# Optimization experiments

Hardware: AMD Instinct MI355X
Metric: run time of the kernel (lower is better)

The kernel has to match this reference:

```python
import jax, jax.numpy as jnp
import numpy as np

EPS = 1e-5  # nn.LayerNorm default

def _ln(x, g, b):
    m = x.mean(-1, keepdims=True)
    v = ((x - m) ** 2).mean(-1, keepdims=True)
    return (x - m) / jnp.sqrt(v + EPS) * g + b


def setup_inputs() -> dict:
    key = jax.random.key(0)
    ks = jax.random.split(key, 16)
    B, T, H, W = 8, 20, 224, 224
    D, NC = 1536, 7
    s = 0.02
    f32 = jnp.float32
    return {
        'x': jax.random.normal(ks[0], (B, 3, T, H, W), f32),
        'timestamp': jax.random.uniform(ks[1], (B,), f32),
        # surrogate backbone: patchify conv (stride 16) + global avg pool -> 1536 feats
        'conv_w': jax.random.normal(ks[2], (D, 3, 16, 16), f32) * s,
        'conv_b': jnp.zeros((D,), f32),
        'w_red': jax.random.normal(ks[3], (D, D), f32) * s,
        'b_red': jnp.zeros((D,), f32),
        'w_num': jax.random.normal(ks[4], (D, 1), f32) * s,
        'b_num': jnp.zeros((D,), f32),
        'time_embed': jax.random.normal(ks[5], (1, T, D), f32) * s,
        'cls_swap': jax.random.normal(ks[6], (1, 5, 1, D), f32) * s,
        'ln_g': jnp.ones((D,), f32),
        'ln_b': jnp.zeros((D,), f32),
        'w_qkv': jax.random.normal(ks[7], (3 * D, D), f32) * s,
        'w_tproj': jax.random.normal(ks[8], (D, D), f32) * s,
        'b_tproj': jnp.zeros((D,), f32),
        'w_tfc': jax.random.normal(ks[9], (D, D), f32) * s,
        'b_tfc': jnp.zeros((D,), f32),
        'w_head': jax.random.normal(ks[10], (NC, D), f32) * s,
        'b_head': jnp.zeros((NC,), f32),
    }


def reference(x, timestamp, conv_w, conv_b, w_red, b_red, w_num, b_num,
              time_embed, cls_swap, ln_g, ln_b, w_qkv, w_tproj, b_tproj,
              w_tfc, b_tfc, w_head, b_head):
    B, C, T, H, W = x.shape
    D = w_red.shape[0]
    NH = 12
    HD = D // NH
    scale = HD ** -0.5

    # (b t) c h w  -> backbone surrogate -> (B*T, D)
    xf = jnp.transpose(x, (0, 2, 1, 3, 4)).reshape(B * T, C, H, W)
    f = jax.lax.conv_general_dilated(
        xf, conv_w, window_strides=(16, 16), padding='VALID',
        dimension_numbers=('NCHW', 'OIHW', 'NCHW'))
    f = (f + conv_b[None, :, None, None]).mean((2, 3))  # global avg pool -> (BT, D)

    xr = (f @ w_red.T + b_red).reshape(B, T, D)           # reduce_dim
    xt = xr + time_embed
    te = timestamp[:, None] @ w_num.T + b_num             # NumberToVector (B, D)
    xt = xt + te[:, None, :]

    # groups: b (n k) c -> b n k c, k=4, n=5; prepend 1 cls token per group
    g = jnp.concatenate(
        [jnp.broadcast_to(cls_swap, (B, 5, 1, D)), xt.reshape(B, 5, 4, D)], axis=2)

    for _ in range(4):  # num_interactions
        gr = g.reshape(B * 5, 5, D)
        hn = _ln(gr, ln_g, ln_b)
        qkv = (hn @ w_qkv.T).reshape(B * 5, 5, 3, NH, HD).transpose(2, 0, 3, 1, 4)
        q, k, v = qkv[0], qkv[1], qkv[2]                  # (b*n, h, t, hd)
        a = jax.nn.softmax(jnp.einsum('bhqd,bhkd->bhqk', q, k) * scale, axis=-1)
        o = jnp.einsum('bhqk,bhkd->bhqd', a, v).transpose(0, 2, 1, 3).reshape(B * 5, 5, D)
        o = o @ w_tproj.T + b_tproj                       # attn proj
        upd = (o @ w_tfc.T + b_tfc) + gr                  # temporal_fc + residual
        g = upd.reshape(B, 5, 5, D)
        # swap cls tokens between groups via roll
        g = g.at[:, :, 0, :].set(jnp.roll(g[:, :, 0, :], 1, axis=1))

    xt = g[:, :, 1:, :].reshape(B, T, D)
    out = xt[:, -1, :] + xr[:, -1, :]
    return out @ w_head.T + b_head  # (B, num_classes)
```

## Files before the change

### kernel.cpp

```cpp
#include <hip/hip_runtime.h>

typedef __attribute__((ext_vector_type(8))) short short8;
typedef __attribute__((ext_vector_type(8))) unsigned short ushort8;
typedef __attribute__((ext_vector_type(4))) float f32x4;
typedef unsigned short ushort_t;

__device__ __forceinline__ ushort_t f2bf(float f) {
    unsigned u = __builtin_bit_cast(unsigned, f);
    u += 0x7fffu + ((u >> 16) & 1u);
    return (ushort_t)(u >> 16);
}
__device__ __forceinline__ float bf2f(ushort_t u) {
    unsigned v = ((unsigned)u) << 16;
    return __builtin_bit_cast(float, v);
}

__device__ __forceinline__ void load_lds16(const void* gp, void* lp) {
    __builtin_amdgcn_global_load_lds(
        (const __attribute__((address_space(1))) void*)gp,
        (__attribute__((address_space(3))) void*)lp, 16, 0, 0);
}

__global__ __launch_bounds__(256, 4) void pool_kernel(
    const float* __restrict__ x, ushort_t* __restrict__ AP) {
    int blk = blockIdx.x, tid = threadIdx.x;
    int bt = blk / 12, rc = blk % 12;
    int c = rc >> 2, igrp = rc & 3;
    int w = tid >> 6, lane = tid & 63;
    int i = igrp * 4 + w;
    int b = bt / 20, t = bt % 20;
    const float* base = x + (size_t)((b * 3 + c) * 20 + t) * 50176;

    f32x4 v[13];
    int ri = (lane >= 56) ? 1 : 0;
    int c4 = lane - 56 * ri;
    #pragma unroll
    for (int it = 0; it < 13; ++it) {
        if (it < 12 || lane < 16)
            v[it] = *(const f32x4*)(base + (16 * ri + i) * 224 + 4 * c4);
        else
            v[it] = (f32x4){0.f, 0.f, 0.f, 0.f};
        ri += 1; c4 += 8;
        if (c4 >= 56) { c4 -= 56; ri += 1; }
    }
    #pragma unroll
    for (int s = 1; s < 13; s <<= 1)
        #pragma unroll
        for (int j = 0; j + s < 13; j += 2 * s)
            v[j] += v[j + s];
    f32x4 acc = v[0];
    #pragma unroll
    for (int m = 4; m <= 32; m <<= 1) {
        acc[0] += __shfl_xor(acc[0], m);
        acc[1] += __shfl_xor(acc[1], m);
        acc[2] += __shfl_xor(acc[2], m);
        acc[3] += __shfl_xor(acc[3], m);
    }
    if (lane < 4) {
        ushort4 o;
        o.x = f2bf(acc[0] * (1.f / 196.f));
        o.y = f2bf(acc[1] * (1.f / 196.f));
        o.z = f2bf(acc[2] * (1.f / 196.f));
        o.w = f2bf(acc[3] * (1.f / 196.f));
        *(ushort4*)(AP + (size_t)bt * 768 + c * 256 + i * 16 + 4 * lane) = o;
    }
}

__global__ __launch_bounds__(256) void wprep_kernel(
    const float* __restrict__ w_qkv, const float* __restrict__ w_tf,
    const float* __restrict__ w_red, const float* __restrict__ conv_w,
    const float* __restrict__ w_tp, const float* __restrict__ b_tp,
    const float* __restrict__ b_tf, const float* __restrict__ cls,
    ushort_t* __restrict__ WQ, ushort_t* __restrict__ WF,
    ushort_t* __restrict__ WR, ushort_t* __restrict__ WCV,
    ushort_t* __restrict__ WTT, float* __restrict__ BC,
    float* __restrict__ GA) {
    __shared__ __align__(16) float smem[64 * 68];
    int blk = blockIdx.x, tid = threadIdx.x;
    if (blk < 6336) {
        long c = (long)blk * 256 + tid;
        const float* s; ushort_t* d; long i;
        if (c < 884736)       { s = w_qkv;  d = WQ;  i = c; }
        else if (c < 1179648) { s = w_tf;   d = WF;  i = c - 884736; }
        else if (c < 1474560) { s = w_red;  d = WR;  i = c - 1179648; }
        else                  { s = conv_w; d = WCV; i = c - 1474560; }
        i <<= 3;
        f32x4 a = *(const f32x4*)(s + i);
        f32x4 b = *(const f32x4*)(s + i + 4);
        ushort8 o;
        o[0] = f2bf(a[0]); o[1] = f2bf(a[1]); o[2] = f2bf(a[2]); o[3] = f2bf(a[3]);
        o[4] = f2bf(b[0]); o[5] = f2bf(b[1]); o[6] = f2bf(b[2]); o[7] = f2bf(b[3]);
        *(ushort8*)(d + i) = o;
    } else if (blk < 6912) {
        int tb = blk - 6336;
        int bi = tb / 24, bj = tb % 24;
        int r0 = (tid >> 4) << 2;
        int c0 = (tid & 15) << 2;
        #pragma unroll
        for (int rr = 0; rr < 4; ++rr) {
            f32x4 v = *(const f32x4*)(w_tp + (size_t)(bi * 64 + r0 + rr) * 1536 + bj * 64 + c0);
            smem[(r0 + rr) * 68 + c0 + 0] = v[0];
            smem[(r0 + rr) * 68 + c0 + 1] = v[1];
            smem[(r0 + rr) * 68 + c0 + 2] = v[2];
            smem[(r0 + rr) * 68 + c0 + 3] = v[3];
        }
        __syncthreads();
        #pragma unroll
        for (int rr = 0; rr < 4; ++rr) {
            int jj = r0 + rr;
            ushort4 o;
            o.x = f2bf(smem[(c0 + 0) * 68 + jj]);
            o.y = f2bf(smem[(c0 + 1) * 68 + jj]);
            o.z = f2bf(smem[(c0 + 2) * 68 + jj]);
            o.w = f2bf(smem[(c0 + 3) * 68 + jj]);
            *(ushort4*)(WTT + (size_t)(bj * 64 + jj) * 1536 + bi * 64 + c0) = o;
        }
    } else if (blk < 6952) {
        int cblk = blk - 6912;
        int b = cblk / 5, n = cblk % 5;
        size_t row = (size_t)(b * 25 + n * 5) * 1536;
        #pragma unroll
        for (int j = 0; j < 6; ++j) {
            int d = tid + j * 256;
            GA[row + d] = cls[n * 1536 + d];
        }
    } else {
        int bb = blk - 6952;
        int row = bb * 16 + (tid >> 4);
        int sub = tid & 15;
        float acc = 0.f;
        for (int j = 0; j < 96; ++j) {
            int k = sub + j * 16;
            acc += w_tf[(size_t)row * 1536 + k] * b_tp[k];
        }
        acc += __shfl_xor(acc, 1); acc += __shfl_xor(acc, 2);
        acc += __shfl_xor(acc, 4); acc += __shfl_xor(acc, 8);
        if (sub == 0) BC[row] = acc + b_tf[row];
    }
}

template <int MT, bool OUT_BF16, bool HAS_BIAS, bool HAS_RES, bool CLS_SWAP, bool BUILD_G>
__global__ __launch_bounds__(64) void gemm_kernel(
    const ushort_t* __restrict__ A, const ushort_t* __restrict__ B,
    void* __restrict__ Cv, const float* __restrict__ bias,
    const float* __restrict__ res, int M, int N, int K,
    float* __restrict__ g_out, const float* __restrict__ temb,
    const float* __restrict__ ts, const float* __restrict__ w_num,
    const float* __restrict__ b_num) {
    constexpr int BUFB = MT * 2048 + 8192;
    __shared__ __align__(16) char lds[2 * BUFB];
    const int lane = threadIdx.x;
    const int tn = blockIdx.x, tm = blockIdx.y;

    f32x4 acc[MT][4];
    #pragma unroll
    for (int m = 0; m < MT; ++m)
        #pragma unroll
        for (int n = 0; n < 4; ++n)
            acc[m][n] = (f32x4){0.f, 0.f, 0.f, 0.f};

    const int nK = K >> 6;
    const int rbase = lane >> 3, cc = lane & 7;

    auto stage = [&](int k0, int buf) {
        char* lA = lds + buf * BUFB;
        char* lB = lA + MT * 2048;
        #pragma unroll
        for (int j = 0; j < MT * 2; ++j) {
            int row = j * 8 + rbase;
            int cf = cc ^ (row & 7);
            int ga = tm * (MT * 16) + row; if (ga > M - 1) ga = M - 1;
            load_lds16(A + (size_t)ga * K + (k0 + cf * 8), lA + j * 1024);
        }
        #pragma unroll
        for (int j = 0; j < 8; ++j) {
            int row = j * 8 + rbase;
            int cf = cc ^ (row & 7);
            load_lds16(B + (size_t)(tn * 64 + row) * K + (k0 + cf * 8), lB + j * 1024);
        }
    };

    stage(0, 0);
    for (int t = 0; t < nK; ++t) {
        int cur = t & 1;
        if (t + 1 < nK) {
            stage((t + 1) << 6, cur ^ 1);
            if constexpr (MT == 2) asm volatile("s_waitcnt vmcnt(12)" ::: "memory");
            else                   asm volatile("s_waitcnt vmcnt(16)" ::: "memory");
        } else {
            asm volatile("s_waitcnt vmcnt(0)" ::: "memory");
        }
        __builtin_amdgcn_sched_barrier(0);
        const char* lA = lds + cur * BUFB;
        const char* lB = lA + MT * 2048;
        #pragma unroll
        for (int ks = 0; ks < 2; ++ks) {
            short8 av[MT], bv[4];
            const int rlo = lane & 15;
            const int chi = ks * 4 + (lane >> 4);
            #pragma unroll
            for (int m = 0; m < MT; ++m) {
                int r = m * 16 + rlo;
                av[m] = *(const short8*)(lA + r * 128 + ((chi ^ (r & 7)) << 4));
            }
            #pragma unroll
            for (int n = 0; n < 4; ++n) {
                int r = n * 16 + rlo;
                bv[n] = *(const short8*)(lB + r * 128 + ((chi ^ (r & 7)) << 4));
            }
            #pragma unroll
            for (int m = 0; m < MT; ++m)
                #pragma unroll
                for (int n = 0; n < 4; ++n)
                    acc[m][n] = __builtin_amdgcn_mfma_f32_16x16x32_bf16(
                        av[m], bv[n], acc[m][n], 0, 0, 0);
        }
    }

    const int c_l = lane & 15, r_q = (lane >> 4) * 4;
    #pragma unroll
    for (int m = 0; m < MT; ++m) {
        #pragma unroll
        for (int reg = 0; reg < 4; ++reg) {
            int r_ = tm * (MT * 16) + m * 16 + r_q + reg;
            if (r_ < M) {
                int r2 = r_;
                if (CLS_SWAP) {
                    int bb = r_ / 25, rem = r_ % 25;
                    if (rem % 5 == 0) r2 = bb * 25 + ((rem / 5 + 1) % 5) * 5;
                }
                #pragma unroll
                for (int n = 0; n < 4; ++n) {
                    int cc_ = tn * 64 + n * 16 + c_l;
                    float v = acc[m][n][reg];
                    if (HAS_BIAS) v += bias[cc_];
                    if (HAS_RES) v += res[(size_t)r_ * N + cc_];
                    if (OUT_BF16) ((ushort_t*)Cv)[(size_t)r2 * N + cc_] = f2bf(v);
                    else          ((float*)Cv)[(size_t)r2 * N + cc_] = v;
                    if (BUILD_G) {
                        int b = r_ / 20, t = r_ % 20;
                        float gval = v + temb[t * 1536 + cc_] +
                                     ts[b] * w_num[cc_] + b_num[cc_];
                        g_out[(size_t)(b * 25 + (t / 4) * 5 + (t % 4) + 1) * 1536 + cc_] = gval;
                    }
                }
            }
        }
    }
}

__global__ __launch_bounds__(256) void ln_kernel(
    const float* __restrict__ g, const float* __restrict__ gamma,
    const float* __restrict__ beta, ushort_t* __restrict__ hn) {
    int r = blockIdx.x, tid = threadIdx.x;
    const float* x = g + (size_t)r * 1536;
    float v[6], s = 0.f, s2 = 0.f;
    #pragma unroll
    for (int j = 0; j < 6; ++j) {
        v[j] = x[tid + j * 256];
        s += v[j]; s2 += v[j] * v[j];
    }
    #pragma unroll
    for (int m = 1; m < 64; m <<= 1) { s += __shfl_xor(s, m); s2 += __shfl_xor(s2, m); }
    __shared__ float red[8];
    int wid = tid >> 6;
    if ((tid & 63) == 0) { red[wid] = s; red[4 + wid] = s2; }
    __syncthreads();
    s  = red[0] + red[1] + red[2] + red[3];
    s2 = red[4] + red[5] + red[6] + red[7];
    float mean = s * (1.0f / 1536.0f);
    float var  = s2 * (1.0f / 1536.0f) - mean * mean;
    float rstd = rsqrtf(var + 1e-5f);
    #pragma unroll
    for (int j = 0; j < 6; ++j) {
        int d = tid + j * 256;
        float y = (v[j] - mean) * rstd * gamma[d] + beta[d];
        hn[(size_t)r * 1536 + d] = f2bf(y);
    }
}

__global__ __launch_bounds__(64) void attn_kernel(const ushort_t* __restrict__ qkv,
                                                  ushort_t* __restrict__ o) {
    int gid = blockIdx.x;
    int h = gid % 12, gg = gid / 12;
    int l = threadIdx.x;
    const ushort_t* basep = qkv + (size_t)gg * 5 * 4608 + h * 128 + 2 * l;
    float q[5][2], k[5][2], v[5][2];
    #pragma unroll
    for (int tt = 0; tt < 5; ++tt) {
        ushort2 qv = *(const ushort2*)(basep + tt * 4608);
        ushort2 kv = *(const ushort2*)(basep + tt * 4608 + 1536);
        ushort2 vv = *(const ushort2*)(basep + tt * 4608 + 3072);
        q[tt][0] = bf2f(qv.x); q[tt][1] = bf2f(qv.y);
        k[tt][0] = bf2f(kv.x); k[tt][1] = bf2f(kv.y);
        v[tt][0] = bf2f(vv.x); v[tt][1] = bf2f(vv.y);
    }
    float sc[5][5];
    #pragma unroll
    for (int i = 0; i < 5; ++i)
        #pragma unroll
        for (int j = 0; j < 5; ++j)
            sc[i][j] = q[i][0] * k[j][0] + q[i][1] * k[j][1];
    #pragma unroll
    for (int m = 1; m < 64; m <<= 1)
        #pragma unroll
        for (int i = 0; i < 5; ++i)
            #pragma unroll
            for (int j = 0; j < 5; ++j)
                sc[i][j] += __shfl_xor(sc[i][j], m);
    const float scale = 0.08838834764831845f;
    float a_[5][5];
    #pragma unroll
    for (int i = 0; i < 5; ++i) {
        float mx = -1e30f;
        #pragma unroll
        for (int j = 0; j < 5; ++j) mx = fmaxf(mx, sc[i][j]);
        float sum = 0.f;
        #pragma unroll
        for (int j = 0; j < 5; ++j) { a_[i][j] = __expf((sc[i][j] - mx) * scale); sum += a_[i][j]; }
        float inv = 1.0f / sum;
        #pragma unroll
        for (int j = 0; j < 5; ++j) a_[i][j] *= inv;
    }
    #pragma unroll
    for (int i = 0; i < 5; ++i) {
        float o0 = 0.f, o1 = 0.f;
        #pragma unroll
        for (int j = 0; j < 5; ++j) { o0 += a_[i][j] * v[j][0]; o1 += a_[i][j] * v[j][1]; }
        ushort2 w; w.x = f2bf(o0); w.y = f2bf(o1);
        *(ushort2*)(o + (size_t)(gg * 5 + i) * 1536 + h * 128 + 2 * l) = w;
    }
}

__global__ __launch_bounds__(64) void head_kernel(
    const float* __restrict__ gfin, const float* __restrict__ xr,
    const float* __restrict__ w_head, const float* __restrict__ b_head,
    float* __restrict__ out) {
    int b = blockIdx.x, l = threadIdx.x;
    const float* gv = gfin + (size_t)(b * 25 + 24) * 1536;
    const float* xv = xr + (size_t)(b * 20 + 19) * 1536;
    float acc[7] = {0, 0, 0, 0, 0, 0, 0};
    for (int d = l; d < 1536; d += 64) {
        float xval = gv[d] + xv[d];
        #pragma unroll
        for (int c = 0; c < 7; ++c) acc[c] += xval * w_head[c * 1536 + d];
    }
    #pragma unroll
    for (int c = 0; c < 7; ++c)
        #pragma unroll
        for (int m = 1; m < 64; m <<= 1) acc[c] += __shfl_xor(acc[c], m);
    if (l == 0) {
        #pragma unroll
        for (int c = 0; c < 7; ++c) out[b * 7 + c] = acc[c] + b_head[c];
    }
}

#define OFF_WQ   0u
#define OFF_WF   14155776u
#define OFF_WR   18874368u
#define OFF_WCV  23592960u
#define OFF_WTT  25952256u
#define OFF_WC   30670848u
#define OFF_BC   35389440u
#define OFF_AP   35395584u
#define OFF_FBF  35641344u
#define OFF_XR   36132864u
#define OFF_GA   37115904u
#define OFF_GB   38344704u
#define OFF_HN   39573504u
#define OFF_QKV  40187904u
#define OFF_OBF  42031104u

extern "C" void kernel_launch(void* const* d_in, const int* in_sizes, int n_in,
                              void* d_out, int out_size, void* d_ws, size_t ws_size,
                              hipStream_t stream) {
    const float* x      = (const float*)d_in[0];
    const float* ts     = (const float*)d_in[1];
    const float* conv_w = (const float*)d_in[2];
    const float* conv_b = (const float*)d_in[3];
    const float* w_red  = (const float*)d_in[4];
    const float* b_red  = (const float*)d_in[5];
    const float* w_num  = (const float*)d_in[6];
    const float* b_num  = (const float*)d_in[7];
    const float* temb   = (const float*)d_in[8];
    const float* cls    = (const float*)d_in[9];
    const float* ln_g   = (const float*)d_in[10];
    const float* ln_b   = (const float*)d_in[11];
    const float* w_qkv  = (const float*)d_in[12];
    const float* w_tp   = (const float*)d_in[13];
    const float* b_tp   = (const float*)d_in[14];
    const float* w_tf   = (const float*)d_in[15];
    const float* b_tf   = (const float*)d_in[16];
    const float* w_head = (const float*)d_in[17];
    const float* b_head = (const float*)d_in[18];

    char* ws = (char*)d_ws;
    ushort_t* WQ  = (ushort_t*)(ws + OFF_WQ);
    ushort_t* WF  = (ushort_t*)(ws + OFF_WF);
    ushort_t* WR  = (ushort_t*)(ws + OFF_WR);
    ushort_t* WCV = (ushort_t*)(ws + OFF_WCV);
    ushort_t* WTT = (ushort_t*)(ws + OFF_WTT);
    ushort_t* WC  = (ushort_t*)(ws + OFF_WC);
    float*    BC  = (float*)(ws + OFF_BC);
    ushort_t* AP  = (ushort_t*)(ws + OFF_AP);
    ushort_t* FBF = (ushort_t*)(ws + OFF_FBF);
    float*    XR  = (float*)(ws + OFF_XR);
    float*    GA  = (float*)(ws + OFF_GA);
    float*    GB  = (float*)(ws + OFF_GB);
    ushort_t* HN  = (ushort_t*)(ws + OFF_HN);
    ushort_t* QKV = (ushort_t*)(ws + OFF_QKV);
    ushort_t* OBF = (ushort_t*)(ws + OFF_OBF);

    pool_kernel<<<1920, 256, 0, stream>>>(x, AP);
    wprep_kernel<<<7048, 256, 0, stream>>>(w_qkv, w_tf, w_red, conv_w, w_tp,
                                           b_tp, b_tf, cls,
                                           WQ, WF, WR, WCV, WTT, BC, GA);
    gemm_kernel<4, true, false, false, false, false><<<dim3(24, 24), 64, 0, stream>>>(
        WF, WTT, WC, nullptr, nullptr, 1536, 1536, 1536,
        nullptr, nullptr, nullptr, nullptr, nullptr);
    gemm_kernel<2, true, true, false, false, false><<<dim3(24, 5), 64, 0, stream>>>(
        AP, WCV, FBF, conv_b, nullptr, 160, 1536, 768,
        nullptr, nullptr, nullptr, nullptr, nullptr);
    gemm_kernel<2, false, true, false, false, true><<<dim3(24, 5), 64, 0, stream>>>(
        FBF, WR, XR, b_red, nullptr, 160, 1536, 1536,
        GA, temb, ts, w_num, b_num);

    float* gsrc = GA;
    float* gdst = GB;
    for (int it = 0; it < 4; ++it) {
        ln_kernel<<<200, 256, 0, stream>>>(gsrc, ln_g, ln_b, HN);
        gemm_kernel<4, true, false, false, false, false><<<dim3(72, 4), 64, 0, stream>>>(
            HN, WQ, QKV, nullptr, nullptr, 200, 4608, 1536,
            nullptr, nullptr, nullptr, nullptr, nullptr);
        attn_kernel<<<480, 64, 0, stream>>>(QKV, OBF);
        gemm_kernel<2, false, true, true, true, false><<<dim3(24, 7), 64, 0, stream>>>(
            OBF, WC, gdst, BC, gsrc, 200, 1536, 1536,
            nullptr, nullptr, nullptr, nullptr, nullptr);
        float* tmp = gsrc; gsrc = gdst; gdst = tmp;
    }
    head_kernel<<<8, 64, 0, stream>>>(gsrc, XR, w_head, b_head, (float*)d_out);
}
```

Before: 231.6 us.

## Split-K the QKV GEMM into two fp32 halves summed in attention

The QKV projection GEMM now splits K=1536 into two halves across twice as many blocks. Each half writes fp32 partial outputs to separate buffers, and the attention kernel loads both and adds them. This doubles the grid of the small-M GEMM to fill more CUs, at the cost of extra fp32 traffic into attention. The pool kernel's load indexing is also rewritten to compute row and column per iteration with a multiply-shift divide.

```diff
diff --git a/kernel.cpp b/kernel.cpp
--- a/kernel.cpp
+++ b/kernel.cpp
@@ -32,16 +32,14 @@
     const float* base = x + (size_t)((b * 3 + c) * 20 + t) * 50176;
 
     f32x4 v[13];
-    int ri = (lane >= 56) ? 1 : 0;
-    int c4 = lane - 56 * ri;
     #pragma unroll
     for (int it = 0; it < 13; ++it) {
-        if (it < 12 || lane < 16)
-            v[it] = *(const f32x4*)(base + (16 * ri + i) * 224 + 4 * c4);
-        else
-            v[it] = (f32x4){0.f, 0.f, 0.f, 0.f};
-        ri += 1; c4 += 8;
-        if (c4 >= 56) { c4 -= 56; ri += 1; }
+        int k = lane + it * 64;
+        int kk = k < 784 ? k : 0;
+        int ri = (kk * 9363) >> 19;
+        int c4 = kk - ri * 56;
+        v[it] = *(const f32x4*)(base + (16 * ri + i) * 224 + 4 * c4);
+        if (k >= 784) v[it] = (f32x4){0.f, 0.f, 0.f, 0.f};
     }
     #pragma unroll
     for (int s = 1; s < 13; s <<= 1)
@@ -139,18 +137,26 @@
     }
 }
 
-template <int MT, bool OUT_BF16, bool HAS_BIAS, bool HAS_RES, bool CLS_SWAP, bool BUILD_G>
+template <int MT, bool OUT_BF16, bool HAS_BIAS, bool HAS_RES, bool CLS_SWAP,
+          bool BUILD_G, bool SPLITK>
 __global__ __launch_bounds__(64) void gemm_kernel(
     const ushort_t* __restrict__ A, const ushort_t* __restrict__ B,
-    void* __restrict__ Cv, const float* __restrict__ bias,
-    const float* __restrict__ res, int M, int N, int K,
+    void* __restrict__ Cv, void* __restrict__ Cv2,
+    const float* __restrict__ bias, const float* __restrict__ res,
+    int M, int N, int K, int KS,
     float* __restrict__ g_out, const float* __restrict__ temb,
     const float* __restrict__ ts, const float* __restrict__ w_num,
     const float* __restrict__ b_num) {
     constexpr int BUFB = MT * 2048 + 8192;
     __shared__ __align__(16) char lds[2 * BUFB];
     const int lane = threadIdx.x;
-    const int tn = blockIdx.x, tm = blockIdx.y;
+    const int tn = blockIdx.x;
+    int tm = blockIdx.y;
+    if (SPLITK) {
+        int half = tm >> 2;
+        tm &= 3;
+        if (half) { A += K; B += K; Cv = Cv2; }
+    }
 
     f32x4 acc[MT][4];
     #pragma unroll
@@ -170,13 +176,13 @@
             int row = j * 8 + rbase;
             int cf = cc ^ (row & 7);
             int ga = tm * (MT * 16) + row; if (ga > M - 1) ga = M - 1;
-            load_lds16(A + (size_t)ga * K + (k0 + cf * 8), lA + j * 1024);
+            load_lds16(A + (size_t)ga * KS + (k0 + cf * 8), lA + j * 1024);
         }
         #pragma unroll
         for (int j = 0; j < 8; ++j) {
             int row = j * 8 + rbase;
             int cf = cc ^ (row & 7);
-            load_lds16(B + (size_t)(tn * 64 + row) * K + (k0 + cf * 8), lB + j * 1024);
+            load_lds16(B + (size_t)(tn * 64 + row) * KS + (k0 + cf * 8), lB + j * 1024);
         }
     };
 
@@ -279,21 +285,27 @@
     }
 }
 
-__global__ __launch_bounds__(64) void attn_kernel(const ushort_t* __restrict__ qkv,
-                                                  ushort_t* __restrict__ o) {
+__global__ __launch_bounds__(64) void attn_kernel(
+    const float* __restrict__ qA, const float* __restrict__ qB,
+    ushort_t* __restrict__ o) {
     int gid = blockIdx.x;
     int h = gid % 12, gg = gid / 12;
     int l = threadIdx.x;
-    const ushort_t* basep = qkv + (size_t)gg * 5 * 4608 + h * 128 + 2 * l;
+    size_t off = (size_t)gg * 5 * 4608 + h * 128 + 2 * l;
+    const float* b0 = qA + off;
+    const float* b1 = qB + off;
     float q[5][2], k[5][2], v[5][2];
     #pragma unroll
     for (int tt = 0; tt < 5; ++tt) {
-        ushort2 qv = *(const ushort2*)(basep + tt * 4608);
-        ushort2 kv = *(const ushort2*)(basep + tt * 4608 + 1536);
-        ushort2 vv = *(const ushort2*)(basep + tt * 4608 + 3072);
-        q[tt][0] = bf2f(qv.x); q[tt][1] = bf2f(qv.y);
-        k[tt][0] = bf2f(kv.x); k[tt][1] = bf2f(kv.y);
-        v[tt][0] = bf2f(vv.x); v[tt][1] = bf2f(vv.y);
+        float2 q0 = *(const float2*)(b0 + tt * 4608);
+        float2 q1 = *(const float2*)(b1 + tt * 4608);
+        float2 k0 = *(const float2*)(b0 + tt * 4608 + 1536);
+        float2 k1 = *(const float2*)(b1 + tt * 4608 + 1536);
+        float2 v0 = *(const float2*)(b0 + tt * 4608 + 3072);
+        float2 v1 = *(const float2*)(b1 + tt * 4608 + 3072);
+        q[tt][0] = q0.x + q1.x; q[tt][1] = q0.y + q1.y;
+        k[tt][0] = k0.x + k1.x; k[tt][1] = k0.y + k1.y;
+        v[tt][0] = v0.x + v1.x; v[tt][1] = v0.y + v1.y;
     }
     float sc[5][5];
     #pragma unroll
@@ -355,21 +367,22 @@
     }
 }
 
-#define OFF_WQ   0u
-#define OFF_WF   14155776u
-#define OFF_WR   18874368u
-#define OFF_WCV  23592960u
-#define OFF_WTT  25952256u
-#define OFF_WC   30670848u
-#define OFF_BC   35389440u
-#define OFF_AP   35395584u
-#define OFF_FBF  35641344u
-#define OFF_XR   36132864u
-#define OFF_GA   37115904u
-#define OFF_GB   38344704u
-#define OFF_HN   39573504u
-#define OFF_QKV  40187904u
-#define OFF_OBF  42031104u
+#define OFF_WQ    0u
+#define OFF_WF    14155776u
+#define OFF_WR    18874368u
+#define OFF_WCV   23592960u
+#define OFF_WTT   25952256u
+#define OFF_WC    30670848u
+#define OFF_BC    35389440u
+#define OFF_AP    35395584u
+#define OFF_FBF   35641344u
+#define OFF_XR    36132864u
+#define OFF_GA    37115904u
+#define OFF_GB    38344704u
+#define OFF_HN    39573504u
+#define OFF_QKV0  40187904u
+#define OFF_QKV1  43874304u
+#define OFF_OBF   47560704u
 
 extern "C" void kernel_launch(void* const* d_in, const int* in_sizes, int n_in,
                               void* d_out, int out_size, void* d_ws, size_t ws_size,
@@ -395,46 +408,47 @@
     const float* b_head = (const float*)d_in[18];
 
     char* ws = (char*)d_ws;
-    ushort_t* WQ  = (ushort_t*)(ws + OFF_WQ);
-    ushort_t* WF  = (ushort_t*)(ws + OFF_WF);
-    ushort_t* WR  = (ushort_t*)(ws + OFF_WR);
-    ushort_t* WCV = (ushort_t*)(ws + OFF_WCV);
-    ushort_t* WTT = (ushort_t*)(ws + OFF_WTT);
-    ushort_t* WC  = (ushort_t*)(ws + OFF_WC);
-    float*    BC  = (float*)(ws + OFF_BC);
-    ushort_t* AP  = (ushort_t*)(ws + OFF_AP);
-    ushort_t* FBF = (ushort_t*)(ws + OFF_FBF);
-    float*    XR  = (float*)(ws + OFF_XR);
-    float*    GA  = (float*)(ws + OFF_GA);
-    float*    GB  = (float*)(ws + OFF_GB);
-    ushort_t* HN  = (ushort_t*)(ws + OFF_HN);
-    ushort_t* QKV = (ushort_t*)(ws + OFF_QKV);
-    ushort_t* OBF = (ushort_t*)(ws + OFF_OBF);
+    ushort_t* WQ   = (ushort_t*)(ws + OFF_WQ);
+    ushort_t* WF   = (ushort_t*)(ws + OFF_WF);
+    ushort_t* WR   = (ushort_t*)(ws + OFF_WR);
+    ushort_t* WCV  = (ushort_t*)(ws + OFF_WCV);
+    ushort_t* WTT  = (ushort_t*)(ws + OFF_WTT);
+    ushort_t* WC   = (ushort_t*)(ws + OFF_WC);
+    float*    BC   = (float*)(ws + OFF_BC);
+    ushort_t* AP   = (ushort_t*)(ws + OFF_AP);
+    ushort_t* FBF  = (ushort_t*)(ws + OFF_FBF);
+    float*    XR   = (float*)(ws + OFF_XR);
+    float*    GA   = (float*)(ws + OFF_GA);
+    float*    GB   = (float*)(ws + OFF_GB);
+    ushort_t* HN   = (ushort_t*)(ws + OFF_HN);
+    float*    QKV0 = (float*)(ws + OFF_QKV0);
+    float*    QKV1 = (float*)(ws + OFF_QKV1);
+    ushort_t* OBF  = (ushort_t*)(ws + OFF_OBF);
 
     pool_kernel<<<1920, 256, 0, stream>>>(x, AP);
     wprep_kernel<<<7048, 256, 0, stream>>>(w_qkv, w_tf, w_red, conv_w, w_tp,
                                            b_tp, b_tf, cls,
                                            WQ, WF, WR, WCV, WTT, BC, GA);
-    gemm_kernel<4, true, false, false, false, false><<<dim3(24, 24), 64, 0, stream>>>(
-        WF, WTT, WC, nullptr, nullptr, 1536, 1536, 1536,
+    gemm_kernel<4, true, false, false, false, false, false><<<dim3(24, 24), 64, 0, stream>>>(
+        WF, WTT, WC, nullptr, nullptr, nullptr, 1536, 1536, 1536, 1536,
         nullptr, nullptr, nullptr, nullptr, nullptr);
-    gemm_kernel<2, true, true, false, false, false><<<dim3(24, 5), 64, 0, stream>>>(
-        AP, WCV, FBF, conv_b, nullptr, 160, 1536, 768,
+    gemm_kernel<2, true, true, false, false, false, false><<<dim3(24, 5), 64, 0, stream>>>(
+        AP, WCV, FBF, nullptr, conv_b, nullptr, 160, 1536, 768, 768,
         nullptr, nullptr, nullptr, nullptr, nullptr);
-    gemm_kernel<2, false, true, false, false, true><<<dim3(24, 5), 64, 0, stream>>>(
-        FBF, WR, XR, b_red, nullptr, 160, 1536, 1536,
+    gemm_kernel<2, false, true, false, false, true, false><<<dim3(24, 5), 64, 0, stream>>>(
+        FBF, WR, XR, nullptr, b_red, nullptr, 160, 1536, 1536, 1536,
         GA, temb, ts, w_num, b_num);
 
     float* gsrc = GA;
     float* gdst = GB;
     for (int it = 0; it < 4; ++it) {
         ln_kernel<<<200, 256, 0, stream>>>(gsrc, ln_g, ln_b, HN);
-        gemm_kernel<4, true, false, false, false, false><<<dim3(72, 4), 64, 0, stream>>>(
-            HN, WQ, QKV, nullptr, nullptr, 200, 4608, 1536,
+        gemm_kernel<4, false, false, false, false, false, true><<<dim3(72, 8), 64, 0, stream>>>(
+            HN, WQ, QKV0, QKV1, nullptr, nullptr, 200, 4608, 768, 1536,
             nullptr, nullptr, nullptr, nullptr, nullptr);
-        attn_kernel<<<480, 64, 0, stream>>>(QKV, OBF);
-        gemm_kernel<2, false, true, true, true, false><<<dim3(24, 7), 64, 0, stream>>>(
-            OBF, WC, gdst, BC, gsrc, 200, 1536, 1536,
+        attn_kernel<<<480, 64, 0, stream>>>(QKV0, QKV1, OBF);
+        gemm_kernel<2, false, true, true, true, false, false><<<dim3(24, 7), 64, 0, stream>>>(
+            OBF, WC, gdst, nullptr, BC, gsrc, 200, 1536, 1536, 1536,
             nullptr, nullptr, nullptr, nullptr, nullptr);
         float* tmp = gsrc; gsrc = gdst; gdst = tmp;
     }
```

New measurement: 212.7 us. 1.09x faster.
